# Kernel tuning notes

Measured on AMD Instinct MI355X. Metric: run time of the kernel, lower is better.

Reference implementation:

```python
import jax, jax.numpy as jnp
import numpy as np

B, H, W, C = 32, 32, 32, 256


def setup_inputs() -> dict:
    key = jax.random.key(0)
    k1, k2 = jax.random.split(key)
    feats1 = jax.random.normal(k1, (B, H, W, C), dtype=jnp.float32)
    feats2 = jax.random.normal(k2, (B, H, W, C), dtype=jnp.float32)
    return {"feats1": feats1, "feats2": feats2}


def reference(feats1, feats2):
    # Training path of LocalFeatureLoss (trainflag=True)
    b, h, w, c = feats1.shape
    l = h * w
    q = feats1.reshape(b, l, c)  # queries: (B, l, C)
    p = feats2.reshape(b, l, c)  # preds:   (B, l, C)
    # M[b, a, j] = <p[b,a], q[b,j]>  == fm2 @ fm1.T per batch
    M = jnp.einsum('bac,bjc->baj', p, q)  # (B, l_pred, l_query)
    max1 = jnp.argmax(M, axis=1)  # (B, l_q): best pred index for each query token
    max2 = jnp.argmax(M, axis=2)  # (B, l_p): best query index for each pred token
    # mutual nearest-neighbor check: m[b, j] = max2[b, max1[b, j]]
    m = jnp.take_along_axis(max2, max1, axis=1)  # (B, l_q)
    valid = jnp.arange(l)[None, :] == m          # (B, l_q) bool
    # gather matched pred descriptors and compute per-pair similarity
    matched_p = jnp.take_along_axis(p, max1[..., None], axis=1)  # (B, l_q, C)
    sims = jnp.sum(q * matched_p, axis=-1)                        # (B, l_q)
    cnt = jnp.sum(valid, axis=1).astype(sims.dtype)               # (B,)
    # mean over mutual NN pairs (torch mean over idx1)
    similarity = jnp.sum(jnp.where(valid, sims, 0.0), axis=1) / jnp.maximum(cnt, 1.0)
    return similarity
```

## Files before the change

kernel.cpp:

```cpp
#include <hip/hip_runtime.h>
#include <hip/hip_bf16.h>

#define BATCH 32
#define L 1024
#define CD 256
#define TM 64
#define TN 64
#define NT (L / TN)
#define KC 128
#define RT_PER_B 16
#define SP_LD (CD + 8)
#define SQ_LD (KC + 8)

typedef __bf16 bf16x8 __attribute__((ext_vector_type(8)));
typedef __bf16 bf16x4 __attribute__((ext_vector_type(4)));
typedef float  f32x4  __attribute__((ext_vector_type(4)));

__device__ __forceinline__ unsigned int enc_f32(float f) {
    unsigned int u = __float_as_uint(f);
    return ((int)u < 0) ? ~u : (u | 0x80000000u);
}
__device__ __forceinline__ float dec_f32(unsigned int u) {
    u = (u & 0x80000000u) ? (u & 0x7FFFFFFFu) : ~u;
    return __uint_as_float(u);
}
__device__ __forceinline__ unsigned long long pmax(unsigned long long a, unsigned long long b) {
    return a > b ? a : b;
}
__device__ __forceinline__ bf16x4 cvt4(float4 v) {
    bf16x4 o;
    o[0] = (__bf16)v.x; o[1] = (__bf16)v.y; o[2] = (__bf16)v.z; o[3] = (__bf16)v.w;
    return o;
}

__global__ __launch_bounds__(256) void mm_argmax_kernel(
    const float* __restrict__ qg,
    const float* __restrict__ pg,
    unsigned long long* __restrict__ colpart,
    int* __restrict__ max2)
{
    __shared__ __bf16 sP[TM][SP_LD];
    __shared__ __bf16 sQ[TN][SQ_LD];
    __shared__ unsigned long long sCol[TN];
    __shared__ unsigned long long sRowW[2][TM];

    const int tid = threadIdx.x;
    const int bid = blockIdx.x;
    const int b    = bid & 31;
    const int rt   = bid >> 5;
    const int row0 = rt * TM;

    const int lane = tid & 63;
    const int w    = tid >> 6;
    const int wm   = w >> 1;
    const int wn   = w & 1;
    const int quad = lane >> 4;
    const int l16  = lane & 15;

    const float* pB = pg + ((size_t)b * L + row0) * CD;
    const float* qB = qg + (size_t)b * L * CD;

    const int sr = tid >> 2;
    const int sc = tid & 3;
    {
        const float4* src = (const float4*)(pB + sr * CD);
        #pragma unroll
        for (int i = 0; i < 16; ++i)
            *(bf16x4*)&sP[sr][(sc + i * 4) * 4] = cvt4(src[sc + i * 4]);
    }

    float4 pf[8];
    {
        const float4* src = (const float4*)(qB + (size_t)sr * CD);
        #pragma unroll
        for (int i = 0; i < 8; ++i) pf[i] = src[sc + i * 4];
    }

    unsigned long long rowbest[2][4];
    #pragma unroll
    for (int tm = 0; tm < 2; ++tm)
        #pragma unroll
        for (int r = 0; r < 4; ++r) rowbest[tm][r] = 0ull;
    unsigned long long pend[2] = {0ull, 0ull};

    for (int nt = 0; nt < NT; ++nt) {
        f32x4 acc[2][2];
        #pragma unroll
        for (int tm = 0; tm < 2; ++tm)
            #pragma unroll
            for (int tn = 0; tn < 2; ++tn) acc[tm][tn] = (f32x4){0.f, 0.f, 0.f, 0.f};

        for (int kc = 0; kc < 2; ++kc) {
            if (nt || kc) __syncthreads();
            if (kc == 0 && nt > 0 && wm == 1 && quad == 0) {
                #pragma unroll
                for (int tn = 0; tn < 2; ++tn) {
                    const int c = wn * 32 + tn * 16 + l16;
                    colpart[((size_t)b * RT_PER_B + rt) * L + (nt - 1) * TN + c] =
                        pmax(pend[tn], sCol[c]);
                }
            }
            #pragma unroll
            for (int i = 0; i < 8; ++i)
                *(bf16x4*)&sQ[sr][(sc + i * 4) * 4] = cvt4(pf[i]);
            if (!(nt == NT - 1 && kc == 1)) {
                const int nnt = (kc == 0) ? nt : nt + 1;
                const int nkc = kc ^ 1;
                const float4* src = (const float4*)(qB + (size_t)(nnt * TN + sr) * CD + nkc * KC);
                #pragma unroll
                for (int i = 0; i < 8; ++i) pf[i] = src[sc + i * 4];
            }
            __syncthreads();
            #pragma unroll
            for (int kk = 0; kk < 4; ++kk) {
                const int ka = kc * KC + kk * 32 + quad * 8;
                const int kb = kk * 32 + quad * 8;
                bf16x8 a0 = *(const bf16x8*)&sP[wm * 32 +      l16][ka];
                bf16x8 a1 = *(const bf16x8*)&sP[wm * 32 + 16 + l16][ka];
                bf16x8 b0 = *(const bf16x8*)&sQ[wn * 32 +      l16][kb];
                bf16x8 b1 = *(const bf16x8*)&sQ[wn * 32 + 16 + l16][kb];
                acc[0][0] = __builtin_amdgcn_mfma_f32_16x16x32_bf16(a0, b0, acc[0][0], 0, 0, 0);
                acc[0][1] = __builtin_amdgcn_mfma_f32_16x16x32_bf16(a0, b1, acc[0][1], 0, 0, 0);
                acc[1][0] = __builtin_amdgcn_mfma_f32_16x16x32_bf16(a1, b0, acc[1][0], 0, 0, 0);
                acc[1][1] = __builtin_amdgcn_mfma_f32_16x16x32_bf16(a1, b1, acc[1][1], 0, 0, 0);
            }
        }

        #pragma unroll
        for (int tn = 0; tn < 2; ++tn) {
            const unsigned int jcol = (unsigned int)(nt * TN + wn * 32 + tn * 16 + l16);
            const unsigned long long jpk = (unsigned long long)(unsigned int)(~jcol);
            unsigned long long cbest = 0ull;
            #pragma unroll
            for (int tm = 0; tm < 2; ++tm) {
                #pragma unroll
                for (int r = 0; r < 4; ++r) {
                    const unsigned int e = enc_f32(acc[tm][tn][r]);
                    const unsigned int aidx =
                        (unsigned int)(row0 + wm * 32 + tm * 16 + quad * 4 + r);
                    cbest = pmax(cbest, ((unsigned long long)e << 32) | (unsigned int)(~aidx));
                    rowbest[tm][r] = pmax(rowbest[tm][r], ((unsigned long long)e << 32) | jpk);
                }
            }
            cbest = pmax(cbest, __shfl_xor(cbest, 16));
            cbest = pmax(cbest, __shfl_xor(cbest, 32));
            if (quad == 0) {
                const int c = wn * 32 + tn * 16 + l16;
                if (wm == 0) sCol[c] = cbest;
                else         pend[tn] = cbest;
            }
        }
    }

    __syncthreads();
    if (wm == 1 && quad == 0) {
        #pragma unroll
        for (int tn = 0; tn < 2; ++tn) {
            const int c = wn * 32 + tn * 16 + l16;
            colpart[((size_t)b * RT_PER_B + rt) * L + (NT - 1) * TN + c] =
                pmax(pend[tn], sCol[c]);
        }
    }

    #pragma unroll
    for (int tm = 0; tm < 2; ++tm) {
        #pragma unroll
        for (int r = 0; r < 4; ++r) {
            unsigned long long pk = rowbest[tm][r];
            pk = pmax(pk, __shfl_xor(pk, 1));
            pk = pmax(pk, __shfl_xor(pk, 2));
            pk = pmax(pk, __shfl_xor(pk, 4));
            pk = pmax(pk, __shfl_xor(pk, 8));
            rowbest[tm][r] = pk;
        }
    }
    if (l16 == 0) {
        #pragma unroll
        for (int tm = 0; tm < 2; ++tm)
            #pragma unroll
            for (int r = 0; r < 4; ++r)
                sRowW[wn][wm * 32 + tm * 16 + quad * 4 + r] = rowbest[tm][r];
    }
    __syncthreads();
    if (w == 0) {
        unsigned long long m = pmax(sRowW[0][lane], sRowW[1][lane]);
        max2[(size_t)b * L + row0 + lane] = (int)(~(unsigned int)m);
    }
}

__global__ __launch_bounds__(256) void finalize_kernel(
    const unsigned long long* __restrict__ colpart,
    const int* __restrict__ max2,
    float* __restrict__ out)
{
    __shared__ int sMax2[L];
    __shared__ float sSum[4];
    __shared__ int sCnt[4];
    const int b = blockIdx.x;
    const int tid = threadIdx.x;

    for (int i = tid; i < L; i += 256) sMax2[i] = max2[(size_t)b * L + i];
    __syncthreads();

    float sum = 0.f;
    int cnt = 0;
    #pragma unroll
    for (int i = 0; i < 4; ++i) {
        const int j = tid + i * 256;
        unsigned long long best = 0ull;
        #pragma unroll
        for (int rt = 0; rt < RT_PER_B; ++rt)
            best = pmax(best, colpart[((size_t)b * RT_PER_B + rt) * L + j]);
        const int a = (int)(~(unsigned int)best) & (L - 1);
        const float val = dec_f32((unsigned int)(best >> 32));
        if (sMax2[a] == j) { sum += val; ++cnt; }
    }
    #pragma unroll
    for (int o = 32; o >= 1; o >>= 1) {
        sum += __shfl_down(sum, o);
        cnt += __shfl_down(cnt, o);
    }
    if ((tid & 63) == 0) { sSum[tid >> 6] = sum; sCnt[tid >> 6] = cnt; }
    __syncthreads();
    if (tid == 0) {
        float S = sSum[0] + sSum[1] + sSum[2] + sSum[3];
        int   C = sCnt[0] + sCnt[1] + sCnt[2] + sCnt[3];
        out[b] = S / fmaxf((float)C, 1.0f);
    }
}

extern "C" void kernel_launch(void* const* d_in, const int* in_sizes, int n_in,
                              void* d_out, int out_size, void* d_ws, size_t ws_size,
                              hipStream_t stream) {
    const float* q = (const float*)d_in[0];
    const float* p = (const float*)d_in[1];
    float* out = (float*)d_out;

    unsigned long long* colpart = (unsigned long long*)d_ws;
    int* max2 = (int*)((char*)d_ws + (size_t)BATCH * RT_PER_B * L * sizeof(unsigned long long));

    mm_argmax_kernel<<<BATCH * RT_PER_B, 256, 0, stream>>>(q, p, colpart, max2);
    finalize_kernel<<<BATCH, 256, 0, stream>>>(colpart, max2, out);
}
```

Before: 135.4 us.

## Split column tiles across two blocks per row tile and merge row partials

Each matmul-argmax block now processes half of the query column tiles, doubling the grid to raise occupancy on the GPU. Row argmax results become per-half partials written to a workspace buffer and merged in the finalize kernel. Shared-memory staging is widened to 8-element bf16 stores. The P tile load and conversion are duplicated across the two halves, adding some redundant global reads.

```diff
diff --git a/kernel.cpp b/kernel.cpp
--- a/kernel.cpp
+++ b/kernel.cpp
@@ -6,7 +6,7 @@
 #define CD 256
 #define TM 64
 #define TN 64
-#define NT (L / TN)
+#define NTB 8
 #define KC 128
 #define RT_PER_B 16
 #define SP_LD (CD + 8)
@@ -27,9 +27,10 @@
 __device__ __forceinline__ unsigned long long pmax(unsigned long long a, unsigned long long b) {
     return a > b ? a : b;
 }
-__device__ __forceinline__ bf16x4 cvt4(float4 v) {
-    bf16x4 o;
-    o[0] = (__bf16)v.x; o[1] = (__bf16)v.y; o[2] = (__bf16)v.z; o[3] = (__bf16)v.w;
+__device__ __forceinline__ bf16x8 cvt8(float4 v0, float4 v1) {
+    bf16x8 o;
+    o[0] = (__bf16)v0.x; o[1] = (__bf16)v0.y; o[2] = (__bf16)v0.z; o[3] = (__bf16)v0.w;
+    o[4] = (__bf16)v1.x; o[5] = (__bf16)v1.y; o[6] = (__bf16)v1.z; o[7] = (__bf16)v1.w;
     return o;
 }
 
@@ -37,7 +38,7 @@
     const float* __restrict__ qg,
     const float* __restrict__ pg,
     unsigned long long* __restrict__ colpart,
-    int* __restrict__ max2)
+    unsigned long long* __restrict__ rowpart)
 {
     __shared__ __bf16 sP[TM][SP_LD];
     __shared__ __bf16 sQ[TN][SQ_LD];
@@ -47,8 +48,11 @@
     const int tid = threadIdx.x;
     const int bid = blockIdx.x;
     const int b    = bid & 31;
-    const int rt   = bid >> 5;
+    const int rth  = bid >> 5;
+    const int rt   = rth >> 1;
+    const int h    = rth & 1;
     const int row0 = rt * TM;
+    const int nt0  = h * NTB;
 
     const int lane = tid & 63;
     const int w    = tid >> 6;
@@ -65,15 +69,21 @@
     {
         const float4* src = (const float4*)(pB + sr * CD);
         #pragma unroll
-        for (int i = 0; i < 16; ++i)
-            *(bf16x4*)&sP[sr][(sc + i * 4) * 4] = cvt4(src[sc + i * 4]);
+        for (int i = 0; i < 8; ++i) {
+            const int s0 = 2 * sc + 8 * i;
+            *(bf16x8*)&sP[sr][s0 * 4] = cvt8(src[s0], src[s0 + 1]);
+        }
     }
 
     float4 pf[8];
     {
-        const float4* src = (const float4*)(qB + (size_t)sr * CD);
-        #pragma unroll
-        for (int i = 0; i < 8; ++i) pf[i] = src[sc + i * 4];
+        const float4* src = (const float4*)(qB + (size_t)(nt0 * TN + sr) * CD);
+        #pragma unroll
+        for (int i = 0; i < 4; ++i) {
+            const int s0 = 2 * sc + 8 * i;
+            pf[2 * i]     = src[s0];
+            pf[2 * i + 1] = src[s0 + 1];
+        }
     }
 
     unsigned long long rowbest[2][4];
@@ -83,7 +93,8 @@
         for (int r = 0; r < 4; ++r) rowbest[tm][r] = 0ull;
     unsigned long long pend[2] = {0ull, 0ull};
 
-    for (int nt = 0; nt < NT; ++nt) {
+    for (int t = 0; t < NTB; ++t) {
+        const int nt = nt0 + t;
         f32x4 acc[2][2];
         #pragma unroll
         for (int tm = 0; tm < 2; ++tm)
@@ -91,8 +102,8 @@
             for (int tn = 0; tn < 2; ++tn) acc[tm][tn] = (f32x4){0.f, 0.f, 0.f, 0.f};
 
         for (int kc = 0; kc < 2; ++kc) {
-            if (nt || kc) __syncthreads();
-            if (kc == 0 && nt > 0 && wm == 1 && quad == 0) {
+            if (t || kc) __syncthreads();
+            if (kc == 0 && t > 0 && wm == 1 && quad == 0) {
                 #pragma unroll
                 for (int tn = 0; tn < 2; ++tn) {
                     const int c = wn * 32 + tn * 16 + l16;
@@ -101,14 +112,20 @@
                 }
             }
             #pragma unroll
-            for (int i = 0; i < 8; ++i)
-                *(bf16x4*)&sQ[sr][(sc + i * 4) * 4] = cvt4(pf[i]);
-            if (!(nt == NT - 1 && kc == 1)) {
+            for (int i = 0; i < 4; ++i) {
+                const int s0 = 2 * sc + 8 * i;
+                *(bf16x8*)&sQ[sr][s0 * 4] = cvt8(pf[2 * i], pf[2 * i + 1]);
+            }
+            if (!(t == NTB - 1 && kc == 1)) {
                 const int nnt = (kc == 0) ? nt : nt + 1;
                 const int nkc = kc ^ 1;
                 const float4* src = (const float4*)(qB + (size_t)(nnt * TN + sr) * CD + nkc * KC);
                 #pragma unroll
-                for (int i = 0; i < 8; ++i) pf[i] = src[sc + i * 4];
+                for (int i = 0; i < 4; ++i) {
+                    const int s0 = 2 * sc + 8 * i;
+                    pf[2 * i]     = src[s0];
+                    pf[2 * i + 1] = src[s0 + 1];
+                }
             }
             __syncthreads();
             #pragma unroll
@@ -157,7 +174,7 @@
         #pragma unroll
         for (int tn = 0; tn < 2; ++tn) {
             const int c = wn * 32 + tn * 16 + l16;
-            colpart[((size_t)b * RT_PER_B + rt) * L + (NT - 1) * TN + c] =
+            colpart[((size_t)b * RT_PER_B + rt) * L + (nt0 + NTB - 1) * TN + c] =
                 pmax(pend[tn], sCol[c]);
         }
     }
@@ -184,13 +201,13 @@
     __syncthreads();
     if (w == 0) {
         unsigned long long m = pmax(sRowW[0][lane], sRowW[1][lane]);
-        max2[(size_t)b * L + row0 + lane] = (int)(~(unsigned int)m);
+        rowpart[(((size_t)b * RT_PER_B + rt) * 2 + h) * TM + lane] = m;
     }
 }
 
 __global__ __launch_bounds__(256) void finalize_kernel(
     const unsigned long long* __restrict__ colpart,
-    const int* __restrict__ max2,
+    const unsigned long long* __restrict__ rowpart,
     float* __restrict__ out)
 {
     __shared__ int sMax2[L];
@@ -199,7 +216,12 @@
     const int b = blockIdx.x;
     const int tid = threadIdx.x;
 
-    for (int i = tid; i < L; i += 256) sMax2[i] = max2[(size_t)b * L + i];
+    for (int i = tid; i < L; i += 256) {
+        const int rt = i >> 6, a = i & 63;
+        const size_t base = (((size_t)b * RT_PER_B + rt) * 2) * TM + a;
+        unsigned long long m = pmax(rowpart[base], rowpart[base + TM]);
+        sMax2[i] = (int)(~(unsigned int)m);
+    }
     __syncthreads();
 
     float sum = 0.f;
@@ -237,8 +259,9 @@
     float* out = (float*)d_out;
 
     unsigned long long* colpart = (unsigned long long*)d_ws;
-    int* max2 = (int*)((char*)d_ws + (size_t)BATCH * RT_PER_B * L * sizeof(unsigned long long));
-
-    mm_argmax_kernel<<<BATCH * RT_PER_B, 256, 0, stream>>>(q, p, colpart, max2);
-    finalize_kernel<<<BATCH, 256, 0, stream>>>(colpart, max2, out);
-}
+    unsigned long long* rowpart =
+        (unsigned long long*)((char*)d_ws + (size_t)BATCH * RT_PER_B * L * sizeof(unsigned long long));
+
+    mm_argmax_kernel<<<BATCH * RT_PER_B * 2, 256, 0, stream>>>(q, p, colpart, rowpart);
+    finalize_kernel<<<BATCH, 256, 0, stream>>>(colpart, rowpart, out);
+}
```

Result: no change. 137.5 us (+1.5%).
